# Performance work log

Measured on AMD Instinct MI355X. Metric: run time of the kernel, lower is better.

## Reference

```python
import jax, jax.numpy as jnp
import numpy as np

TOP_K = 2

def setup_inputs() -> dict:
    key = jax.random.key(0)
    k1, k2 = jax.random.split(key)
    N, D, E = 16384, 2048, 64
    x = jax.random.normal(k1, (N, D), dtype=jnp.float32)
    W = jax.random.normal(k2, (D, E), dtype=jnp.float32) * (1.0 / np.sqrt(D))
    b = jnp.zeros((E,), dtype=jnp.float32)
    return {"x": x, "W": W, "b": b}

def reference(x, W, b):
    # gate linear: [N, D] @ [D, E] + [E]
    logits = jnp.einsum('nd,de->ne', x, W) + b
    gates = jax.nn.softmax(logits, axis=-1)
    topk_vals, topk_idx = jax.lax.top_k(gates, TOP_K)  # [N, k]
    N = gates.shape[0]
    rows = jnp.arange(N)[:, None]  # [N, 1] broadcast over k
    dispatch_mask = jnp.zeros_like(gates).at[rows, topk_idx].set(topk_vals)
    return dispatch_mask, topk_idx
```

## Files before the change

### kernel.cpp

```cpp
#include <hip/hip_runtime.h>
#include <math.h>

#define NROWS 16384
#define DDIM  2048
#define EEXP  64
#define RB    64
#define KD    64
#define NCHUNK (DDIM / KD)
#define XSTR  68
#define WSTR  64
#define PSTR  66

#define XOFF(b) ((b) * 4352)
#define WOFF(b) (8704 + (b) * 4096)

#define ROW_FMA(i, XV)                                                        \
    acc[i][0]=fmaf(XV.x,wl0.x,acc[i][0]); acc[i][1]=fmaf(XV.x,wl0.y,acc[i][1]); \
    acc[i][2]=fmaf(XV.x,wl0.z,acc[i][2]); acc[i][3]=fmaf(XV.x,wl0.w,acc[i][3]); \
    acc[i][4]=fmaf(XV.x,wh0.x,acc[i][4]); acc[i][5]=fmaf(XV.x,wh0.y,acc[i][5]); \
    acc[i][6]=fmaf(XV.x,wh0.z,acc[i][6]); acc[i][7]=fmaf(XV.x,wh0.w,acc[i][7]); \
    acc[i][0]=fmaf(XV.y,wl1.x,acc[i][0]); acc[i][1]=fmaf(XV.y,wl1.y,acc[i][1]); \
    acc[i][2]=fmaf(XV.y,wl1.z,acc[i][2]); acc[i][3]=fmaf(XV.y,wl1.w,acc[i][3]); \
    acc[i][4]=fmaf(XV.y,wh1.x,acc[i][4]); acc[i][5]=fmaf(XV.y,wh1.y,acc[i][5]); \
    acc[i][6]=fmaf(XV.y,wh1.z,acc[i][6]); acc[i][7]=fmaf(XV.y,wh1.w,acc[i][7]); \
    acc[i][0]=fmaf(XV.z,wl2.x,acc[i][0]); acc[i][1]=fmaf(XV.z,wl2.y,acc[i][1]); \
    acc[i][2]=fmaf(XV.z,wl2.z,acc[i][2]); acc[i][3]=fmaf(XV.z,wl2.w,acc[i][3]); \
    acc[i][4]=fmaf(XV.z,wh2.x,acc[i][4]); acc[i][5]=fmaf(XV.z,wh2.y,acc[i][5]); \
    acc[i][6]=fmaf(XV.z,wh2.z,acc[i][6]); acc[i][7]=fmaf(XV.z,wh2.w,acc[i][7]); \
    acc[i][0]=fmaf(XV.w,wl3.x,acc[i][0]); acc[i][1]=fmaf(XV.w,wl3.y,acc[i][1]); \
    acc[i][2]=fmaf(XV.w,wl3.z,acc[i][2]); acc[i][3]=fmaf(XV.w,wl3.w,acc[i][3]); \
    acc[i][4]=fmaf(XV.w,wh3.x,acc[i][4]); acc[i][5]=fmaf(XV.w,wh3.y,acc[i][5]); \
    acc[i][6]=fmaf(XV.w,wh3.z,acc[i][6]); acc[i][7]=fmaf(XV.w,wh3.w,acc[i][7]);

#define GROUP(d0)                                                             \
    {                                                                         \
        float4 xv0 = *(const float4*)(xb + 0*544 + (d0));                     \
        float4 xv1 = *(const float4*)(xb + 1*544 + (d0));                     \
        float4 xv2 = *(const float4*)(xb + 2*544 + (d0));                     \
        float4 xv3 = *(const float4*)(xb + 3*544 + (d0));                     \
        float4 xv4 = *(const float4*)(xb + 4*544 + (d0));                     \
        float4 xv5 = *(const float4*)(xb + 5*544 + (d0));                     \
        float4 xv6 = *(const float4*)(xb + 6*544 + (d0));                     \
        float4 xv7 = *(const float4*)(xb + 7*544 + (d0));                     \
        float4 wl0 = *(const float4*)(wb + ((d0)+0)*WSTR);                    \
        float4 wh0 = *(const float4*)(wb + ((d0)+0)*WSTR + 4);                \
        float4 wl1 = *(const float4*)(wb + ((d0)+1)*WSTR);                    \
        float4 wh1 = *(const float4*)(wb + ((d0)+1)*WSTR + 4);                \
        float4 wl2 = *(const float4*)(wb + ((d0)+2)*WSTR);                    \
        float4 wh2 = *(const float4*)(wb + ((d0)+2)*WSTR + 4);                \
        float4 wl3 = *(const float4*)(wb + ((d0)+3)*WSTR);                    \
        float4 wh3 = *(const float4*)(wb + ((d0)+3)*WSTR + 4);                \
        ROW_FMA(0, xv0) ROW_FMA(1, xv1) ROW_FMA(2, xv2) ROW_FMA(3, xv3)       \
        ROW_FMA(4, xv4) ROW_FMA(5, xv5) ROW_FMA(6, xv6) ROW_FMA(7, xv7)       \
    }

__global__ __launch_bounds__(512, 2)
void router_kernel(const float* __restrict__ x,
                   const float* __restrict__ W,
                   const float* __restrict__ bias_v,
                   float* __restrict__ mask_out,
                   float* __restrict__ idx_out) {
    __shared__ __align__(16) float smem[16896];

    const int tid  = threadIdx.x;
    const int lane = tid & 63;
    const int wave = __builtin_amdgcn_readfirstlane(tid >> 6);
    const int eg   = lane & 7;
    const int rg   = lane >> 3;
    const int row0 = blockIdx.x * RB;
    const int dw   = wave * 8;

    float acc[8][8];
#pragma unroll
    for (int i = 0; i < 8; ++i)
#pragma unroll
        for (int e = 0; e < 8; ++e) acc[i][e] = 0.0f;

    {
        const int f0 = tid, f1 = tid + 512;
        float4 vx0 = *(const float4*)(x + (size_t)(row0 + (f0 >> 4)) * DDIM + (f0 & 15) * 4);
        float4 vx1 = *(const float4*)(x + (size_t)(row0 + (f1 >> 4)) * DDIM + (f1 & 15) * 4);
        float4 vw0 = *(const float4*)(W + (size_t)(f0 >> 4) * EEXP + (f0 & 15) * 4);
        float4 vw1 = *(const float4*)(W + (size_t)(f1 >> 4) * EEXP + (f1 & 15) * 4);
        *(float4*)(smem + XOFF(0) + (f0 >> 4) * XSTR + (f0 & 15) * 4) = vx0;
        *(float4*)(smem + XOFF(0) + (f1 >> 4) * XSTR + (f1 & 15) * 4) = vx1;
        *(float4*)(smem + WOFF(0) + (f0 >> 4) * WSTR + (f0 & 15) * 4) = vw0;
        *(float4*)(smem + WOFF(0) + (f1 >> 4) * WSTR + (f1 & 15) * 4) = vw1;
    }

#pragma unroll 1
    for (int c = 0; c < NCHUNK; ++c) {
        const int buf = c & 1;
        const bool more = (c + 1) < NCHUNK;
        float4 vx0, vx1, vw0, vw1;
        if (more) {
            const int f0 = tid, f1 = tid + 512;
            const int cb = (c + 1) * KD;
            vx0 = *(const float4*)(x + (size_t)(row0 + (f0 >> 4)) * DDIM + cb + (f0 & 15) * 4);
            vx1 = *(const float4*)(x + (size_t)(row0 + (f1 >> 4)) * DDIM + cb + (f1 & 15) * 4);
            vw0 = *(const float4*)(W + (size_t)(cb + (f0 >> 4)) * EEXP + (f0 & 15) * 4);
            vw1 = *(const float4*)(W + (size_t)(cb + (f1 >> 4)) * EEXP + (f1 & 15) * 4);
        }
        __syncthreads();

        const float* xb = smem + XOFF(buf) + rg * XSTR;
        const float* wb = smem + WOFF(buf) + eg * 8;
        GROUP(dw)
        GROUP(dw + 4)

        if (more) {
            const int nb = buf ^ 1;
            const int f0 = tid, f1 = tid + 512;
            *(float4*)(smem + XOFF(nb) + (f0 >> 4) * XSTR + (f0 & 15) * 4) = vx0;
            *(float4*)(smem + XOFF(nb) + (f1 >> 4) * XSTR + (f1 & 15) * 4) = vx1;
            *(float4*)(smem + WOFF(nb) + (f0 >> 4) * WSTR + (f0 & 15) * 4) = vw0;
            *(float4*)(smem + WOFF(nb) + (f1 >> 4) * WSTR + (f1 & 15) * 4) = vw1;
        }
    }

    const float bias = bias_v[lane];
#pragma unroll
    for (int h = 0; h < 2; ++h) {
        __syncthreads();
#pragma unroll
        for (int ii = 0; ii < 4; ++ii) {
            const int i  = 4 * h + ii;
            const int rp = rg + 8 * i - 32 * h;
            float* pb = smem + wave * 2112 + rp * PSTR + eg * 8;
            *(float2*)(pb + 0) = make_float2(acc[i][0], acc[i][1]);
            *(float2*)(pb + 2) = make_float2(acc[i][2], acc[i][3]);
            *(float2*)(pb + 4) = make_float2(acc[i][4], acc[i][5]);
            *(float2*)(pb + 6) = make_float2(acc[i][6], acc[i][7]);
        }
        __syncthreads();
#pragma unroll
        for (int rr = 0; rr < 4; ++rr) {
            const int rp  = wave * 4 + rr;
            const int row = row0 + 32 * h + rp;
            float logit = bias;
#pragma unroll
            for (int p = 0; p < 8; ++p) logit += smem[p * 2112 + rp * PSTR + lane];

            float m = logit;
#pragma unroll
            for (int off = 32; off >= 1; off >>= 1)
                m = fmaxf(m, __shfl_xor(m, off));
            float ex = __expf(logit - m);
            float s = ex;
#pragma unroll
            for (int off = 32; off >= 1; off >>= 1)
                s += __shfl_xor(s, off);
            float gate = ex / s;

            float v1 = logit; int i1 = lane;
#pragma unroll
            for (int off = 32; off >= 1; off >>= 1) {
                float ov = __shfl_xor(v1, off);
                int   oi = __shfl_xor(i1, off);
                if (ov > v1 || (ov == v1 && oi < i1)) { v1 = ov; i1 = oi; }
            }
            float v2 = (lane == i1) ? -INFINITY : logit; int i2 = lane;
#pragma unroll
            for (int off = 32; off >= 1; off >>= 1) {
                float ov = __shfl_xor(v2, off);
                int   oi = __shfl_xor(i2, off);
                if (ov > v2 || (ov == v2 && oi < i2)) { v2 = ov; i2 = oi; }
            }

            float outv = (lane == i1 || lane == i2) ? gate : 0.0f;
            mask_out[(size_t)row * EEXP + lane] = outv;
            if (lane == 0) {
                idx_out[row * 2 + 0] = (float)i1;
                idx_out[row * 2 + 1] = (float)i2;
            }
        }
    }
}

extern "C" void kernel_launch(void* const* d_in, const int* in_sizes, int n_in,
                              void* d_out, int out_size, void* d_ws, size_t ws_size,
                              hipStream_t stream) {
    const float* x = (const float*)d_in[0];
    const float* W = (const float*)d_in[1];
    const float* b = (const float*)d_in[2];
    float* mask_out = (float*)d_out;
    float* idx_out  = mask_out + (size_t)NROWS * EEXP;

    dim3 grid(NROWS / RB);
    dim3 block(512);
    router_kernel<<<grid, block, 0, stream>>>(x, W, b, mask_out, idx_out);
}
```

Before: 216.7 us.

## Use bf16x3 split MFMA for gate GEMM with swizzled LDS weight tiles

Replaces the FP32 FMA-based GEMM with MFMA 32x32x16 bf16 instructions. Each fp32 value is split into three bf16 parts, and six cross-term products are accumulated to keep near-fp32 accuracy. X is loaded straight into registers and converted there, while W is converted to its three bf16 levels into double-buffered, XOR-swizzled LDS tiles with a K chunk of 128. Each wave handles a K-slice, and the per-wave partials are reduced through LDS in the existing epilogue. The change trades scalar FMA throughput for matrix-core throughput plus conversion overhead and a larger LDS footprint of 96KB. That footprint may limit occupancy to fewer blocks per CU.

```diff
diff --git a/kernel.cpp b/kernel.cpp
--- a/kernel.cpp
+++ b/kernel.cpp
@@ -5,54 +5,41 @@
 #define DDIM  2048
 #define EEXP  64
 #define RB    64
-#define KD    64
-#define NCHUNK (DDIM / KD)
-#define XSTR  68
-#define WSTR  64
-#define PSTR  66
-
-#define XOFF(b) ((b) * 4352)
-#define WOFF(b) (8704 + (b) * 4096)
-
-#define ROW_FMA(i, XV)                                                        \
-    acc[i][0]=fmaf(XV.x,wl0.x,acc[i][0]); acc[i][1]=fmaf(XV.x,wl0.y,acc[i][1]); \
-    acc[i][2]=fmaf(XV.x,wl0.z,acc[i][2]); acc[i][3]=fmaf(XV.x,wl0.w,acc[i][3]); \
-    acc[i][4]=fmaf(XV.x,wh0.x,acc[i][4]); acc[i][5]=fmaf(XV.x,wh0.y,acc[i][5]); \
-    acc[i][6]=fmaf(XV.x,wh0.z,acc[i][6]); acc[i][7]=fmaf(XV.x,wh0.w,acc[i][7]); \
-    acc[i][0]=fmaf(XV.y,wl1.x,acc[i][0]); acc[i][1]=fmaf(XV.y,wl1.y,acc[i][1]); \
-    acc[i][2]=fmaf(XV.y,wl1.z,acc[i][2]); acc[i][3]=fmaf(XV.y,wl1.w,acc[i][3]); \
-    acc[i][4]=fmaf(XV.y,wh1.x,acc[i][4]); acc[i][5]=fmaf(XV.y,wh1.y,acc[i][5]); \
-    acc[i][6]=fmaf(XV.y,wh1.z,acc[i][6]); acc[i][7]=fmaf(XV.y,wh1.w,acc[i][7]); \
-    acc[i][0]=fmaf(XV.z,wl2.x,acc[i][0]); acc[i][1]=fmaf(XV.z,wl2.y,acc[i][1]); \
-    acc[i][2]=fmaf(XV.z,wl2.z,acc[i][2]); acc[i][3]=fmaf(XV.z,wl2.w,acc[i][3]); \
-    acc[i][4]=fmaf(XV.z,wh2.x,acc[i][4]); acc[i][5]=fmaf(XV.z,wh2.y,acc[i][5]); \
-    acc[i][6]=fmaf(XV.z,wh2.z,acc[i][6]); acc[i][7]=fmaf(XV.z,wh2.w,acc[i][7]); \
-    acc[i][0]=fmaf(XV.w,wl3.x,acc[i][0]); acc[i][1]=fmaf(XV.w,wl3.y,acc[i][1]); \
-    acc[i][2]=fmaf(XV.w,wl3.z,acc[i][2]); acc[i][3]=fmaf(XV.w,wl3.w,acc[i][3]); \
-    acc[i][4]=fmaf(XV.w,wh3.x,acc[i][4]); acc[i][5]=fmaf(XV.w,wh3.y,acc[i][5]); \
-    acc[i][6]=fmaf(XV.w,wh3.z,acc[i][6]); acc[i][7]=fmaf(XV.w,wh3.w,acc[i][7]);
-
-#define GROUP(d0)                                                             \
-    {                                                                         \
-        float4 xv0 = *(const float4*)(xb + 0*544 + (d0));                     \
-        float4 xv1 = *(const float4*)(xb + 1*544 + (d0));                     \
-        float4 xv2 = *(const float4*)(xb + 2*544 + (d0));                     \
-        float4 xv3 = *(const float4*)(xb + 3*544 + (d0));                     \
-        float4 xv4 = *(const float4*)(xb + 4*544 + (d0));                     \
-        float4 xv5 = *(const float4*)(xb + 5*544 + (d0));                     \
-        float4 xv6 = *(const float4*)(xb + 6*544 + (d0));                     \
-        float4 xv7 = *(const float4*)(xb + 7*544 + (d0));                     \
-        float4 wl0 = *(const float4*)(wb + ((d0)+0)*WSTR);                    \
-        float4 wh0 = *(const float4*)(wb + ((d0)+0)*WSTR + 4);                \
-        float4 wl1 = *(const float4*)(wb + ((d0)+1)*WSTR);                    \
-        float4 wh1 = *(const float4*)(wb + ((d0)+1)*WSTR + 4);                \
-        float4 wl2 = *(const float4*)(wb + ((d0)+2)*WSTR);                    \
-        float4 wh2 = *(const float4*)(wb + ((d0)+2)*WSTR + 4);                \
-        float4 wl3 = *(const float4*)(wb + ((d0)+3)*WSTR);                    \
-        float4 wh3 = *(const float4*)(wb + ((d0)+3)*WSTR + 4);                \
-        ROW_FMA(0, xv0) ROW_FMA(1, xv1) ROW_FMA(2, xv2) ROW_FMA(3, xv3)       \
-        ROW_FMA(4, xv4) ROW_FMA(5, xv5) ROW_FMA(6, xv6) ROW_FMA(7, xv7)       \
-    }
+#define KC    128
+#define NCH   (DDIM / KC)
+
+#define LVL      16384
+#define WBUFO(b) ((b) * 49152)
+
+typedef short  bf16x8 __attribute__((ext_vector_type(8)));
+typedef float  f32x16 __attribute__((ext_vector_type(16)));
+
+union V4 { uint4 u; bf16x8 s; };
+
+static __device__ __forceinline__ void split3x2(float f0, float f1,
+                                                unsigned int &p0, unsigned int &p1,
+                                                unsigned int &p2) {
+    unsigned int a0 = __float_as_uint(f0), b0 = __float_as_uint(f1);
+    unsigned int ah = a0 & 0xffff0000u,   bh = b0 & 0xffff0000u;
+    float fa1 = f0 - __uint_as_float(ah);
+    float fb1 = f1 - __uint_as_float(bh);
+    unsigned int a1 = __float_as_uint(fa1), b1 = __float_as_uint(fb1);
+    unsigned int am = a1 & 0xffff0000u,     bm = b1 & 0xffff0000u;
+    float fa2 = fa1 - __uint_as_float(am);
+    float fb2 = fb1 - __uint_as_float(bm);
+    p0 = (a0 >> 16) | bh;
+    p1 = (a1 >> 16) | bm;
+    p2 = (__float_as_uint(fa2) >> 16) | (__float_as_uint(fb2) & 0xffff0000u);
+}
+
+static __device__ __forceinline__ void cvt8(float4 u, float4 v, V4 &q0, V4 &q1, V4 &q2) {
+    split3x2(u.x, u.y, q0.u.x, q1.u.x, q2.u.x);
+    split3x2(u.z, u.w, q0.u.y, q1.u.y, q2.u.y);
+    split3x2(v.x, v.y, q0.u.z, q1.u.z, q2.u.z);
+    split3x2(v.z, v.w, q0.u.w, q1.u.w, q2.u.w);
+}
+
+#define MM(ACC, A, B) ACC = __builtin_amdgcn_mfma_f32_32x32x16_bf16((A), (B), ACC, 0, 0, 0)
 
 __global__ __launch_bounds__(512, 2)
 void router_kernel(const float* __restrict__ x,
@@ -60,96 +47,134 @@
                    const float* __restrict__ bias_v,
                    float* __restrict__ mask_out,
                    float* __restrict__ idx_out) {
-    __shared__ __align__(16) float smem[16896];
+    __shared__ __align__(16) unsigned char smem[98304];
 
     const int tid  = threadIdx.x;
     const int lane = tid & 63;
-    const int wave = __builtin_amdgcn_readfirstlane(tid >> 6);
-    const int eg   = lane & 7;
-    const int rg   = lane >> 3;
+    const int w    = __builtin_amdgcn_readfirstlane(tid >> 6);
     const int row0 = blockIdx.x * RB;
-    const int dw   = wave * 8;
-
-    float acc[8][8];
-#pragma unroll
-    for (int i = 0; i < 8; ++i)
-#pragma unroll
-        for (int e = 0; e < 8; ++e) acc[i][e] = 0.0f;
-
+    const int l31  = lane & 31;
+    const int h    = lane >> 5;
+
+    const float* xp0 = x + (size_t)(row0 + l31) * DDIM + (w * 16 + h * 8);
+    const float* xp1 = xp0 + (size_t)32 * DDIM;
+
+    const int eW = lane;
+    const float* wq0 = W + (size_t)(w * 8) * EEXP + eW;
+    const float* wq1 = W + (size_t)((w + 8) * 8) * EEXP + eW;
+    const int wb0 = eW * 256 + ((w * 16)       ^ ((eW & 7) << 4));
+    const int wb1 = eW * 256 + (((w + 8) * 16) ^ ((eW & 7) << 4));
+
+    const int koff = w * 32 + h * 16;
+    const int be0  = l31 * 256        + (koff ^ ((l31 & 7) << 4));
+    const int be1  = (l31 + 32) * 256 + (koff ^ ((l31 & 7) << 4));
+
+    f32x16 acc0, acc1, acc2, acc3;
+#pragma unroll
+    for (int i = 0; i < 16; ++i) { acc0[i] = 0.f; acc1[i] = 0.f; acc2[i] = 0.f; acc3[i] = 0.f; }
+
+    float wr0[8], wr1[8];
+#pragma unroll
+    for (int j = 0; j < 8; ++j) {
+        wr0[j] = wq0[(size_t)j * EEXP];
+        wr1[j] = wq1[(size_t)j * EEXP];
+    }
     {
-        const int f0 = tid, f1 = tid + 512;
-        float4 vx0 = *(const float4*)(x + (size_t)(row0 + (f0 >> 4)) * DDIM + (f0 & 15) * 4);
-        float4 vx1 = *(const float4*)(x + (size_t)(row0 + (f1 >> 4)) * DDIM + (f1 & 15) * 4);
-        float4 vw0 = *(const float4*)(W + (size_t)(f0 >> 4) * EEXP + (f0 & 15) * 4);
-        float4 vw1 = *(const float4*)(W + (size_t)(f1 >> 4) * EEXP + (f1 & 15) * 4);
-        *(float4*)(smem + XOFF(0) + (f0 >> 4) * XSTR + (f0 & 15) * 4) = vx0;
-        *(float4*)(smem + XOFF(0) + (f1 >> 4) * XSTR + (f1 & 15) * 4) = vx1;
-        *(float4*)(smem + WOFF(0) + (f0 >> 4) * WSTR + (f0 & 15) * 4) = vw0;
-        *(float4*)(smem + WOFF(0) + (f1 >> 4) * WSTR + (f1 & 15) * 4) = vw1;
-    }
+        unsigned char* d = smem + WBUFO(0);
+        V4 q0, q1, q2;
+        cvt8(make_float4(wr0[0],wr0[1],wr0[2],wr0[3]),
+             make_float4(wr0[4],wr0[5],wr0[6],wr0[7]), q0, q1, q2);
+        *(uint4*)(d + wb0) = q0.u; *(uint4*)(d + LVL + wb0) = q1.u; *(uint4*)(d + 2*LVL + wb0) = q2.u;
+        cvt8(make_float4(wr1[0],wr1[1],wr1[2],wr1[3]),
+             make_float4(wr1[4],wr1[5],wr1[6],wr1[7]), q0, q1, q2);
+        *(uint4*)(d + wb1) = q0.u; *(uint4*)(d + LVL + wb1) = q1.u; *(uint4*)(d + 2*LVL + wb1) = q2.u;
+    }
+    float4 xa00 = *(const float4*)(xp0);
+    float4 xa01 = *(const float4*)(xp0 + 4);
+    float4 xa10 = *(const float4*)(xp1);
+    float4 xa11 = *(const float4*)(xp1 + 4);
+    __syncthreads();
 
 #pragma unroll 1
-    for (int c = 0; c < NCHUNK; ++c) {
-        const int buf = c & 1;
-        const bool more = (c + 1) < NCHUNK;
-        float4 vx0, vx1, vw0, vw1;
+    for (int c = 0; c < NCH; ++c) {
+        const int  buf  = c & 1;
+        const bool more = (c + 1) < NCH;
+
         if (more) {
-            const int f0 = tid, f1 = tid + 512;
-            const int cb = (c + 1) * KD;
-            vx0 = *(const float4*)(x + (size_t)(row0 + (f0 >> 4)) * DDIM + cb + (f0 & 15) * 4);
-            vx1 = *(const float4*)(x + (size_t)(row0 + (f1 >> 4)) * DDIM + cb + (f1 & 15) * 4);
-            vw0 = *(const float4*)(W + (size_t)(cb + (f0 >> 4)) * EEXP + (f0 & 15) * 4);
-            vw1 = *(const float4*)(W + (size_t)(cb + (f1 >> 4)) * EEXP + (f1 & 15) * 4);
+            const float* q0p = wq0 + (size_t)(c + 1) * KC * EEXP;
+            const float* q1p = wq1 + (size_t)(c + 1) * KC * EEXP;
+#pragma unroll
+            for (int j = 0; j < 8; ++j) { wr0[j] = q0p[(size_t)j * EEXP]; wr1[j] = q1p[(size_t)j * EEXP]; }
+        }
+
+        V4 a00, a10, a20, a01, a11, a21;
+        cvt8(xa00, xa01, a00, a10, a20);
+        cvt8(xa10, xa11, a01, a11, a21);
+
+        if (more) {
+            xa00 = *(const float4*)(xp0 + (c + 1) * KC);
+            xa01 = *(const float4*)(xp0 + (c + 1) * KC + 4);
+            xa10 = *(const float4*)(xp1 + (c + 1) * KC);
+            xa11 = *(const float4*)(xp1 + (c + 1) * KC + 4);
+        }
+
+        const unsigned char* wB = smem + WBUFO(buf);
+        bf16x8 b00 = *(const bf16x8*)(wB + be0);
+        bf16x8 b01 = *(const bf16x8*)(wB + be1);
+        bf16x8 b10 = *(const bf16x8*)(wB + LVL + be0);
+        bf16x8 b11 = *(const bf16x8*)(wB + LVL + be1);
+        bf16x8 b20 = *(const bf16x8*)(wB + 2 * LVL + be0);
+        bf16x8 b21 = *(const bf16x8*)(wB + 2 * LVL + be1);
+
+        MM(acc0, a00.s, b00); MM(acc1, a00.s, b01); MM(acc2, a01.s, b00); MM(acc3, a01.s, b01);
+        MM(acc0, a00.s, b10); MM(acc1, a00.s, b11); MM(acc2, a01.s, b10); MM(acc3, a01.s, b11);
+        MM(acc0, a10.s, b00); MM(acc1, a10.s, b01); MM(acc2, a11.s, b00); MM(acc3, a11.s, b01);
+        MM(acc0, a00.s, b20); MM(acc1, a00.s, b21); MM(acc2, a01.s, b20); MM(acc3, a01.s, b21);
+        MM(acc0, a10.s, b10); MM(acc1, a10.s, b11); MM(acc2, a11.s, b10); MM(acc3, a11.s, b11);
+        MM(acc0, a20.s, b00); MM(acc1, a20.s, b01); MM(acc2, a21.s, b00); MM(acc3, a21.s, b01);
+
+        if (more) {
+            unsigned char* d = smem + WBUFO(buf ^ 1);
+            V4 q0, q1, q2;
+            cvt8(make_float4(wr0[0],wr0[1],wr0[2],wr0[3]),
+                 make_float4(wr0[4],wr0[5],wr0[6],wr0[7]), q0, q1, q2);
+            *(uint4*)(d + wb0) = q0.u; *(uint4*)(d + LVL + wb0) = q1.u; *(uint4*)(d + 2*LVL + wb0) = q2.u;
+            cvt8(make_float4(wr1[0],wr1[1],wr1[2],wr1[3]),
+                 make_float4(wr1[4],wr1[5],wr1[6],wr1[7]), q0, q1, q2);
+            *(uint4*)(d + wb1) = q0.u; *(uint4*)(d + LVL + wb1) = q1.u; *(uint4*)(d + 2*LVL + wb1) = q2.u;
         }
         __syncthreads();
-
-        const float* xb = smem + XOFF(buf) + rg * XSTR;
-        const float* wb = smem + WOFF(buf) + eg * 8;
-        GROUP(dw)
-        GROUP(dw + 4)
-
-        if (more) {
-            const int nb = buf ^ 1;
-            const int f0 = tid, f1 = tid + 512;
-            *(float4*)(smem + XOFF(nb) + (f0 >> 4) * XSTR + (f0 & 15) * 4) = vx0;
-            *(float4*)(smem + XOFF(nb) + (f1 >> 4) * XSTR + (f1 & 15) * 4) = vx1;
-            *(float4*)(smem + WOFF(nb) + (f0 >> 4) * WSTR + (f0 & 15) * 4) = vw0;
-            *(float4*)(smem + WOFF(nb) + (f1 >> 4) * WSTR + (f1 & 15) * 4) = vw1;
-        }
     }
 
     const float bias = bias_v[lane];
-#pragma unroll
-    for (int h = 0; h < 2; ++h) {
+    float* ep = (float*)smem;
+#pragma unroll
+    for (int ph = 0; ph < 2; ++ph) {
         __syncthreads();
 #pragma unroll
-        for (int ii = 0; ii < 4; ++ii) {
-            const int i  = 4 * h + ii;
-            const int rp = rg + 8 * i - 32 * h;
-            float* pb = smem + wave * 2112 + rp * PSTR + eg * 8;
-            *(float2*)(pb + 0) = make_float2(acc[i][0], acc[i][1]);
-            *(float2*)(pb + 2) = make_float2(acc[i][2], acc[i][3]);
-            *(float2*)(pb + 4) = make_float2(acc[i][4], acc[i][5]);
-            *(float2*)(pb + 6) = make_float2(acc[i][6], acc[i][7]);
+        for (int r = 0; r < 16; ++r) {
+            const int rowl = (r & 3) + 8 * (r >> 2) + 4 * h;
+            const float va = (ph == 0) ? acc0[r] : acc2[r];
+            const float vb = (ph == 0) ? acc1[r] : acc3[r];
+            ep[w * 2048 + rowl * 64 + l31]      = va;
+            ep[w * 2048 + rowl * 64 + l31 + 32] = vb;
         }
         __syncthreads();
 #pragma unroll
         for (int rr = 0; rr < 4; ++rr) {
-            const int rp  = wave * 4 + rr;
-            const int row = row0 + 32 * h + rp;
+            const int rl  = w * 4 + rr;
+            const int row = row0 + ph * 32 + rl;
             float logit = bias;
 #pragma unroll
-            for (int p = 0; p < 8; ++p) logit += smem[p * 2112 + rp * PSTR + lane];
+            for (int p = 0; p < 8; ++p) logit += ep[p * 2048 + rl * 64 + lane];
 
             float m = logit;
 #pragma unroll
-            for (int off = 32; off >= 1; off >>= 1)
-                m = fmaxf(m, __shfl_xor(m, off));
+            for (int off = 32; off >= 1; off >>= 1) m = fmaxf(m, __shfl_xor(m, off));
             float ex = __expf(logit - m);
             float s = ex;
 #pragma unroll
-            for (int off = 32; off >= 1; off >>= 1)
-                s += __shfl_xor(s, off);
+            for (int off = 32; off >= 1; off >>= 1) s += __shfl_xor(s, off);
             float gate = ex / s;
 
             float v1 = logit; int i1 = lane;
```

New measurement: 219.9 us. About the same (+1.5%).
